# Performance work log

Hardware: AMD Instinct MI355X
Metric: run time of the kernel (lower is better)

## Reference

```python
import jax, jax.numpy as jnp
import numpy as np

FRAME_PERIOD = 80
SAMPLE_RATE = 16000
FFT_LENGTH = 1024
HALF = FFT_LENGTH // 2 + 1
DEFAULT_F0 = 500.0
Q1 = -0.15
F_MIN = 3.0 * SAMPLE_RATE / (FFT_LENGTH - 3)
DF = SAMPLE_RATE / FFT_LENGTH  # Hz per bin
TAU = 2.0 * np.pi
EPS32 = float(np.finfo(np.float32).eps)
# static max mirroring boundary for linear smoothing (max width = 2/3*default_f0)
BPAD = int(DEFAULT_F0 * (2.0 / 3.0) / DF) + 2


def _interp(c, pos):
    """Linear interpolation of c along last axis at fractional positions pos."""
    L = c.shape[-1]
    i0 = jnp.clip(jnp.floor(pos).astype(jnp.int32), 0, L - 2)
    w = pos - i0.astype(pos.dtype)
    c0 = jnp.take_along_axis(c, i0, axis=-1)
    c1 = jnp.take_along_axis(c, i0 + 1, axis=-1)
    return c0 + (c1 - c0) * w


def _cheaptrick(x, f0):
    B, T = x.shape
    N = f0.shape[-1]
    f0 = jnp.where(f0 <= F_MIN, DEFAULT_F0, f0)[..., None]  # [B,N,1]

    # --- get_windowed_waveform (pitch-synchronous Hanning, ratio=3, bias=0) ---
    base = jnp.arange(FFT_LENGTH) - FFT_LENGTH // 2              # [F]
    centers = jnp.arange(N)[:, None] * FRAME_PERIOD             # [N,1]
    idx = jnp.clip(centers + base[None, :], 0, T - 1)           # [N,F] safe indices
    seg = x[:, idx]                                             # [B,N,F]
    half_win = jnp.round(1.5 * SAMPLE_RATE / f0)                # [B,N,1]
    basef = base.astype(x.dtype)
    window = 0.5 + 0.5 * jnp.cos(jnp.pi * basef * f0 / (1.5 * SAMPLE_RATE))
    window = window * (jnp.abs(basef) <= half_win)              # [B,N,F]
    wav = seg * window
    # remove weighted mean (WORLD GetWindowedWaveform)
    wav = wav - window * (wav.sum(-1, keepdims=True) / window.sum(-1, keepdims=True))
    # power normalization
    wav = wav / jnp.sqrt(jnp.sum(wav * wav, -1, keepdims=True) + 1e-12)

    # --- power spectrum ---
    ps = jnp.abs(jnp.fft.rfft(wav, FFT_LENGTH)) ** 2            # [B,N,HALF]

    # --- DC correction: mirror spectrum around f0 below f0 ---
    ramp = jnp.arange(HALF, dtype=ps.dtype)
    center_bin = f0 * (FFT_LENGTH / SAMPLE_RATE)                # fractional bin of f0
    replica = _interp(ps, jnp.clip(center_bin - ramp, 0.0, HALF - 1.0))
    ps = ps + replica * (ramp < jnp.floor(center_bin) + 1.0)

    # --- linear smoothing with width = 2/3 * f0 (rectangular moving average) ---
    width = f0 * (2.0 / 3.0)                                    # Hz, [B,N,1]
    mir = jnp.pad(ps, ((0, 0), (0, 0), (BPAD, BPAD)), mode="reflect")
    cum = jnp.cumsum(mir, axis=-1) * DF                         # [B,N,HALF+2*BPAD]
    wb = width / DF                                             # width in bins
    p_low = ramp - 0.5 * wb + (BPAD - 0.5)
    ps = (_interp(cum, p_low + wb) - _interp(cum, p_low)) / width

    # infinitesimal noise floor (torch.randn_like(..).abs() * eps)
    noise = jnp.abs(jax.random.normal(jax.random.key(1234), ps.shape, ps.dtype)) * EPS32
    ps = ps + noise

    # --- cepstral liftering ---
    quef = ramp / SAMPLE_RATE                                   # quefrency [HALF]
    z = f0 * quef                                               # [B,N,HALF]
    lifter = jnp.sinc(z).at[..., 0].set(1.0) * (1.0 - 2.0 * Q1 + 2.0 * Q1 * jnp.cos(TAU * z))
    cep = jnp.fft.irfft(jnp.log(ps), FFT_LENGTH)[..., :HALF]
    # hfft(c) == irfft(conj(c), n) * n ; c is real here
    logps = (jnp.fft.irfft(cep * lifter, FFT_LENGTH) * FFT_LENGTH)[..., :HALF]
    return logps


def setup_inputs() -> dict:
    key = jax.random.key(0)
    k1, k2 = jax.random.split(key)
    B, N = 4, 5000
    T = N * FRAME_PERIOD
    x = jax.random.normal(k1, (B, T), dtype=jnp.float32)
    f0 = jax.random.randint(k2, (B, N), 0, 400).astype(jnp.float32)
    return {"x": x, "f0": f0}


def reference(x, f0):
    return _cheaptrick(x, f0)
```

## Files before the change

### kernel.cpp

```cpp
#include <hip/hip_runtime.h>
#include <math.h>


constexpr int   NFFT  = 1024;
constexpr int   HALFB = 513;
constexpr int   NMIR  = 559;
constexpr float DF    = 15.625f;
constexpr float PI_F  = 3.14159274101257324f;
constexpr float NOISE_C = 9.5113724e-8f;


__device__ inline void fft_stage1_cplx_reg(
    const float x0r, const float x0i, const float x1r, const float x1i,
    const float x2r, const float x2i, const float x3r, const float x3i,
    float* __restrict__ qr, float* __restrict__ qi,
    const float* __restrict__ ctab, const int tid)
{
  const float t0r = x0r + x2r, t0i = x0i + x2i;
  const float t1r = x0r - x2r, t1i = x0i - x2i;
  const float t2r = x1r + x3r, t2i = x1i + x3i;
  const float t3r = x1r - x3r, t3i = x1i - x3i;
  const float y0r = t0r + t2r, y0i = t0i + t2i;
  const float y1r = t1r + t3i, y1i = t1i - t3r;
  const float y2r = t0r - t2r, y2i = t0i - t2i;
  const float y3r = t1r - t3i, y3i = t1i + t3r;
  const float c1 = ctab[tid],     s1 = ctab[tid + 768];
  const float c2 = ctab[2 * tid], s2 = ctab[(2 * tid + 768) & 1023];
  const float c3 = ctab[3 * tid], s3 = ctab[(3 * tid + 768) & 1023];
  reinterpret_cast<float4*>(qr)[tid] = make_float4(
      y0r, y1r * c1 + y1i * s1, y2r * c2 + y2i * s2, y3r * c3 + y3i * s3);
  reinterpret_cast<float4*>(qi)[tid] = make_float4(
      y0i, y1i * c1 - y1r * s1, y2i * c2 - y2r * s2, y3i * c3 - y3r * s3);
  __syncthreads();
}

__device__ inline void fft_stage1_cplx(const float* __restrict__ pr,
                                       const float* __restrict__ pi_,
                                       float* __restrict__ qr,
                                       float* __restrict__ qi,
                                       const float* __restrict__ ctab,
                                       const int tid)
{
  fft_stage1_cplx_reg(pr[tid],       pi_[tid],       pr[tid + 256], pi_[tid + 256],
                      pr[tid + 512], pi_[tid + 512], pr[tid + 768], pi_[tid + 768],
                      qr, qi, ctab, tid);
}

#define R4_LOAD_BFLY(pr, pi_)                                   \
  const float x0r = pr[tid      ], x0i = pi_[tid      ];        \
  const float x1r = pr[tid + 256], x1i = pi_[tid + 256];        \
  const float x2r = pr[tid + 512], x2i = pi_[tid + 512];        \
  const float x3r = pr[tid + 768], x3i = pi_[tid + 768];        \
  const float t0r = x0r + x2r, t0i = x0i + x2i;                 \
  const float t1r = x0r - x2r, t1i = x0i - x2i;                 \
  const float t2r = x1r + x3r, t2i = x1i + x3i;                 \
  const float t3r = x1r - x3r, t3i = x1i - x3i;

__device__ inline void fft_stage4(const float* __restrict__ pr,
                                  const float* __restrict__ pi_,
                                  float* __restrict__ qr,
                                  float* __restrict__ qi,
                                  const float* __restrict__ ctab,
                                  const int lg2s, const int tid)
{
  R4_LOAD_BFLY(pr, pi_)
  const float y0r = t0r + t2r, y0i = t0i + t2i;
  const float y1r = t1r + t3i, y1i = t1i - t3r;
  const float y2r = t0r - t2r, y2i = t0i - t2i;
  const float y3r = t1r - t3i, y3i = t1i + t3r;
  const int s  = 1 << lg2s;
  const int q  = tid & (s - 1);
  const int tw = tid - q;
  const float c1 = ctab[tw],     s1 = ctab[tw + 768];
  const float c2 = ctab[2 * tw], s2 = ctab[(2 * tw + 768) & 1023];
  const float c3 = ctab[3 * tw], s3 = ctab[(3 * tw + 768) & 1023];
  const int o0 = 3 * tw + tid;
  qr[o0]         = y0r;
  qi[o0]         = y0i;
  qr[o0 + s]     = y1r * c1 + y1i * s1;
  qi[o0 + s]     = y1i * c1 - y1r * s1;
  qr[o0 + 2 * s] = y2r * c2 + y2i * s2;
  qi[o0 + 2 * s] = y2i * c2 - y2r * s2;
  qr[o0 + 3 * s] = y3r * c3 + y3i * s3;
  qi[o0 + 3 * s] = y3i * c3 - y3r * s3;
  __syncthreads();
}

__device__ inline void fft_stage4_final(const float* __restrict__ pr,
                                        const float* __restrict__ pi_,
                                        float* __restrict__ qr,
                                        float* __restrict__ qi,
                                        const int tid)
{
  R4_LOAD_BFLY(pr, pi_)
  qr[tid]       = t0r + t2r;  qi[tid]       = t0i + t2i;
  qr[tid + 256] = t1r + t3i;  qi[tid + 256] = t1i - t3r;
  qr[tid + 512] = t0r - t2r;  qi[tid + 512] = t0i - t2i;
  qr[tid + 768] = t1r - t3i;  qi[tid + 768] = t1i + t3r;
  __syncthreads();
}

__device__ inline void unpack_ps(const float* __restrict__ Zr,
                                 const float* __restrict__ Zi,
                                 float* __restrict__ pA,
                                 float* __restrict__ pB,
                                 const int tid)
{
#pragma unroll
  for (int j = 0; j < 2; ++j) {
    const int k  = tid + 256 * j;
    const int mk = (NFFT - k) & (NFFT - 1);
    const float zr = Zr[k], zi = Zi[k];
    const float wr = Zr[mk], wi = Zi[mk];
    const float ar = 0.5f * (zr + wr), ai = 0.5f * (zi - wi);
    const float nr = zr - wr,          ni = zi + wi;
    pA[k] = ar * ar + ai * ai;
    pB[k] = 0.25f * (ni * ni + nr * nr);
  }
  if (tid == 0) {
    const float zr = Zr[512], zi = Zi[512];
    pA[512] = zr * zr;
    pB[512] = zi * zi;
  }
  __syncthreads();
}

__device__ inline float lifter_val(const float f0, const int k)
{
  if (k == 0) return 1.0f;
  const float z = f0 * ((float)k * (1.0f / 16000.0f));
  return (sinpif(z) / (PI_F * z)) * (1.3f - 0.3f * cospif(2.0f * z));
}

__device__ inline void fft_final_lifter2(const float* __restrict__ pr,
                                         const float* __restrict__ pi_,
                                         float* __restrict__ cr,
                                         float* __restrict__ ci,
                                         const float f0A, const float f0B,
                                         const int tid)
{
  R4_LOAD_BFLY(pr, pi_)
  const float y0r = t0r + t2r, y0i = t0i + t2i;
  const float y1r = t1r + t3i, y1i = t1i - t3r;
  const float vA0 = (y0r * (1.0f / 1024.0f)) * lifter_val(f0A, tid);
  const float vB0 = (y0i * (1.0f / 1024.0f)) * lifter_val(f0B, tid);
  const float vA1 = (y1r * (1.0f / 1024.0f)) * lifter_val(f0A, tid + 256);
  const float vB1 = (y1i * (1.0f / 1024.0f)) * lifter_val(f0B, tid + 256);
  cr[tid] = vA0;  ci[tid] = vB0;
  if (tid >= 1) { cr[1024 - tid] = vA0;  ci[1024 - tid] = vB0; }
  cr[tid + 256] = vA1;  ci[tid + 256] = vB1;
  cr[768 - tid] = vA1;  ci[768 - tid] = vB1;
  if (tid == 0) {
    const float y2r = t0r - t2r, y2i = t0i - t2i;
    cr[512] = (y2r * (1.0f / 1024.0f)) * lifter_val(f0A, 512);
    ci[512] = (y2i * (1.0f / 1024.0f)) * lifter_val(f0B, 512);
  }
  __syncthreads();
}

__device__ inline void fft_final_store2(const float* __restrict__ pr,
                                        const float* __restrict__ pi_,
                                        float* __restrict__ oA,
                                        float* __restrict__ oB,
                                        const int tid)
{
  R4_LOAD_BFLY(pr, pi_)
  oA[tid]       = t0r + t2r;   oB[tid]       = t0i + t2i;
  oA[tid + 256] = t1r + t3i;   oB[tid + 256] = t1i - t3r;
  if (tid == 0) { oA[512] = t0r - t2r;  oB[512] = t0i - t2i; }
}

template<int M>
__device__ inline void block_sum_multi(float* v, float* red, const int tid)
{
#pragma unroll
  for (int c = 0; c < M; ++c) {
    float s = v[c];
#pragma unroll
    for (int o = 32; o > 0; o >>= 1) s += __shfl_down(s, o, 64);
    v[c] = s;
  }
  const int lane = tid & 63, w = tid >> 6;
  __syncthreads();
  if (lane == 0) {
#pragma unroll
    for (int c = 0; c < M; ++c) red[w * M + c] = v[c];
  }
  __syncthreads();
#pragma unroll
  for (int c = 0; c < M; ++c)
    v[c] = red[c] + red[M + c] + red[2 * M + c] + red[3 * M + c];
}

__device__ inline int reflect_idx(int i)
{
  int j = i - 23;
  if (j < 0)   j = -j;
  if (j > 512) j = 1024 - j;
  return j;
}

__device__ inline float interp_cum(const float* c, float pos)
{
  int i0 = (int)floorf(pos);
  i0 = min(max(i0, 0), NMIR - 2);
  const float w  = pos - (float)i0;
  const float c0 = c[i0];
  return c0 + (c[i0 + 1] - c0) * w;
}

__device__ inline void cumsum559_dual(const float* __restrict__ srcA,
                                      const float* __restrict__ srcB,
                                      float* __restrict__ dstA,
                                      float* __restrict__ dstB,
                                      float* red, const int tid)
{
  const int g = tid >> 7;
  const int l = tid & 127;
  const float* src = g ? srcB : srcA;
  float*       dst = g ? dstB : dstA;
  const int base = l * 5;
  float a[5];
  float run = 0.f;
#pragma unroll
  for (int i = 0; i < 5; ++i) {
    a[i] = (base + i < NMIR) ? src[reflect_idx(base + i)] : 0.f;
    run += a[i];
  }
  float v = run;
  const int lane = tid & 63;
  const int wv = tid >> 6;
#pragma unroll
  for (int o = 1; o < 64; o <<= 1) {
    const float t2 = __shfl_up(v, o, 64);
    if (lane >= o) v += t2;
  }
  __syncthreads();
  if (lane == 63) red[wv] = v;
  __syncthreads();
  const float woff = (wv & 1) ? red[wv - 1] : 0.f;
  float c = (v - run) + woff;
#pragma unroll
  for (int i = 0; i < 5; ++i) {
    c += a[i];
    if (base + i < NMIR) dst[base + i] = c * DF;
  }
  __syncthreads();
}

__global__ __launch_bounds__(256)
void cheaptrick_kernel(const float* __restrict__ x, const float* __restrict__ f0g,
                       float* __restrict__ out, const int N, const int T)
{
  __shared__ float ctab[1024];
  __shared__ __align__(16) float Ar[1024];
  __shared__ __align__(16) float Ai[1024];
  __shared__ __align__(16) float Br[1024];
  __shared__ __align__(16) float Bi[1024];
  __shared__ float red[16];

  const int tid = threadIdx.x;
  const int NP  = N >> 1;
  const int b   = blockIdx.x / NP;
  const int p   = blockIdx.x - b * NP;
  const int n0  = 2 * p;
  const int fidA = b * N + n0;

  for (int m = tid; m < 1024; m += 256)
    ctab[m] = cospif((float)m * (1.0f / 512.0f));

  float f0A = f0g[fidA], f0B = f0g[fidA + 1];
  if (f0A <= 47.0127335f) f0A = 500.0f;
  if (f0B <= 47.0127335f) f0B = 500.0f;

  const float hwA = rintf(24000.0f / f0A);
  const float hwB = rintf(24000.0f / f0B);
  const float* xb = x + (size_t)b * T;
  const int cA = n0 * 80, cB = cA + 80;

  float wavA[4], winA[4], wavB[4], winB[4];
  float sums[4] = {0.f, 0.f, 0.f, 0.f};
#pragma unroll
  for (int j = 0; j < 4; ++j) {
    const int t = tid + j * 256;
    const float basef = (float)(t - 512);
    const int ia = min(max(cA + t - 512, 0), T - 1);
    const int ib = min(max(cB + t - 512, 0), T - 1);
    const float sa = xb[ia], sb = xb[ib];
    float wA = 0.5f + 0.5f * cospif(basef * f0A * (1.0f / 24000.0f));
    wA = (fabsf(basef) <= hwA) ? wA : 0.0f;
    float wB = 0.5f + 0.5f * cospif(basef * f0B * (1.0f / 24000.0f));
    wB = (fabsf(basef) <= hwB) ? wB : 0.0f;
    winA[j] = wA;  wavA[j] = sa * wA;
    winB[j] = wB;  wavB[j] = sb * wB;
    sums[0] += wavA[j];  sums[1] += wA;
    sums[2] += wavB[j];  sums[3] += wB;
  }
  block_sum_multi<4>(sums, red, tid);
  const float cmA = sums[0] / sums[1];
  const float cmB = sums[2] / sums[3];
  float sq[2] = {0.f, 0.f};
#pragma unroll
  for (int j = 0; j < 4; ++j) {
    wavA[j] -= winA[j] * cmA;  sq[0] += wavA[j] * wavA[j];
    wavB[j] -= winB[j] * cmB;  sq[1] += wavB[j] * wavB[j];
  }
  block_sum_multi<2>(sq, red, tid);
  const float invA = 1.0f / sqrtf(sq[0] + 1e-12f);
  const float invB = 1.0f / sqrtf(sq[1] + 1e-12f);

  fft_stage1_cplx_reg(wavA[0] * invA, wavB[0] * invB,
                      wavA[1] * invA, wavB[1] * invB,
                      wavA[2] * invA, wavB[2] * invB,
                      wavA[3] * invA, wavB[3] * invB, Br, Bi, ctab, tid);
  fft_stage4(Br, Bi, Ar, Ai, ctab, 2, tid);
  fft_stage4(Ar, Ai, Br, Bi, ctab, 4, tid);
  fft_stage4(Br, Bi, Ar, Ai, ctab, 6, tid);
  fft_stage4_final(Ar, Ai, Br, Bi, tid);

  unpack_ps(Br, Bi, Ar, Ai, tid);

  if (tid < 128) {
    const int k = tid & 63;
    float* P = (tid < 64) ? Ar : Ai;
    const float f = (tid < 64) ? f0A : f0B;
    const float cb  = f * 0.064f;
    const float thr = floorf(cb) + 1.0f;
    if ((float)k < thr) {
      const float pos = fminf(cb - (float)k, 512.0f);
      const int i0 = min((int)pos, 511);
      const float w  = pos - (float)i0;
      const float r0 = P[i0], r1 = P[i0 + 1];
      P[k] += r0 + (r1 - r0) * w;
    }
  }
  __syncthreads();

  cumsum559_dual(Ar, Ai, Br, Bi, red, tid);

  const float wdA = f0A * (float)(2.0 / 3.0), wbA = wdA / DF;
  const float wdB = f0B * (float)(2.0 / 3.0), wbB = wdB / DF;
  for (int k = tid; k < HALFB; k += 256) {
    const float plA = ((float)k - 0.5f * wbA) + 22.5f;
    const float lgA =
        logf((interp_cum(Br, plA + wbA) - interp_cum(Br, plA)) / wdA + NOISE_C);
    const float plB = ((float)k - 0.5f * wbB) + 22.5f;
    const float lgB =
        logf((interp_cum(Bi, plB + wbB) - interp_cum(Bi, plB)) / wdB + NOISE_C);
    Ar[k] = lgA;  Ai[k] = lgB;
    if (k >= 1 && k <= 511) { Ar[NFFT - k] = lgA;  Ai[NFFT - k] = lgB; }
  }
  __syncthreads();

  fft_stage1_cplx(Ar, Ai, Br, Bi, ctab, tid);
  fft_stage4(Br, Bi, Ar, Ai, ctab, 2, tid);
  fft_stage4(Ar, Ai, Br, Bi, ctab, 4, tid);
  fft_stage4(Br, Bi, Ar, Ai, ctab, 6, tid);
  fft_final_lifter2(Ar, Ai, Br, Bi, f0A, f0B, tid);

  fft_stage1_cplx(Br, Bi, Ar, Ai, ctab, tid);
  fft_stage4(Ar, Ai, Br, Bi, ctab, 2, tid);
  fft_stage4(Br, Bi, Ar, Ai, ctab, 4, tid);
  fft_stage4(Ar, Ai, Br, Bi, ctab, 6, tid);
  fft_final_store2(Br, Bi,
                   out + (size_t)fidA * HALFB,
                   out + (size_t)(fidA + 1) * HALFB, tid);
}

extern "C" void kernel_launch(void* const* d_in, const int* in_sizes, int n_in,
                              void* d_out, int out_size, void* d_ws, size_t ws_size,
                              hipStream_t stream)
{
  (void)n_in; (void)out_size; (void)d_ws; (void)ws_size;
  const float* x   = (const float*)d_in[0];
  const float* f0  = (const float*)d_in[1];
  float*       out = (float*)d_out;

  const int B  = 4;
  const int BN = in_sizes[1];
  const int N  = BN / B;
  const int T  = in_sizes[0] / B;

  hipLaunchKernelGGL(cheaptrick_kernel, dim3(BN / 2), dim3(256), 0, stream,
                     x, f0, out, N, T);
}
```

Measured before the change: 186.3 us.

## Store FFT buffers and twiddles as interleaved complex pairs in LDS

Switches the shared-memory FFT workspaces from split real/imag float arrays to interleaved float2 complex arrays, and stores the twiddle table as (cos, sin) pairs. Each butterfly load becomes one 64-bit LDS access instead of two 32-bit ones, and each twiddle needs one paired read instead of two separate table reads. The scratch real-valued buffers for power spectrum and cumulative sum are aliased into the complex buffers. The trade-off is a different bank-access pattern for 8-byte LDS accesses, and possible extra register shuffling for the vector types.

```diff
diff --git a/kernel.cpp b/kernel.cpp
--- a/kernel.cpp
+++ b/kernel.cpp
@@ -1,6 +1,9 @@
 #include <hip/hip_runtime.h>
 #include <math.h>
 
+
+typedef float v2f __attribute__((ext_vector_type(2)));
+typedef float v4f __attribute__((ext_vector_type(4)));
 
 constexpr int   NFFT  = 1024;
 constexpr int   HALFB = 513;
@@ -9,118 +12,84 @@
 constexpr float PI_F  = 3.14159274101257324f;
 constexpr float NOISE_C = 9.5113724e-8f;
 
-
-__device__ inline void fft_stage1_cplx_reg(
-    const float x0r, const float x0i, const float x1r, const float x1i,
-    const float x2r, const float x2i, const float x3r, const float x3i,
-    float* __restrict__ qr, float* __restrict__ qi,
-    const float* __restrict__ ctab, const int tid)
-{
-  const float t0r = x0r + x2r, t0i = x0i + x2i;
-  const float t1r = x0r - x2r, t1i = x0i - x2i;
-  const float t2r = x1r + x3r, t2i = x1i + x3i;
-  const float t3r = x1r - x3r, t3i = x1i - x3i;
-  const float y0r = t0r + t2r, y0i = t0i + t2i;
-  const float y1r = t1r + t3i, y1i = t1i - t3r;
-  const float y2r = t0r - t2r, y2i = t0i - t2i;
-  const float y3r = t1r - t3i, y3i = t1i + t3r;
-  const float c1 = ctab[tid],     s1 = ctab[tid + 768];
-  const float c2 = ctab[2 * tid], s2 = ctab[(2 * tid + 768) & 1023];
-  const float c3 = ctab[3 * tid], s3 = ctab[(3 * tid + 768) & 1023];
-  reinterpret_cast<float4*>(qr)[tid] = make_float4(
-      y0r, y1r * c1 + y1i * s1, y2r * c2 + y2i * s2, y3r * c3 + y3i * s3);
-  reinterpret_cast<float4*>(qi)[tid] = make_float4(
-      y0i, y1i * c1 - y1r * s1, y2i * c2 - y2r * s2, y3i * c3 - y3r * s3);
-  __syncthreads();
-}
-
-__device__ inline void fft_stage1_cplx(const float* __restrict__ pr,
-                                       const float* __restrict__ pi_,
-                                       float* __restrict__ qr,
-                                       float* __restrict__ qi,
-                                       const float* __restrict__ ctab,
-                                       const int tid)
-{
-  fft_stage1_cplx_reg(pr[tid],       pi_[tid],       pr[tid + 256], pi_[tid + 256],
-                      pr[tid + 512], pi_[tid + 512], pr[tid + 768], pi_[tid + 768],
-                      qr, qi, ctab, tid);
-}
-
-#define R4_LOAD_BFLY(pr, pi_)                                   \
-  const float x0r = pr[tid      ], x0i = pi_[tid      ];        \
-  const float x1r = pr[tid + 256], x1i = pi_[tid + 256];        \
-  const float x2r = pr[tid + 512], x2i = pi_[tid + 512];        \
-  const float x3r = pr[tid + 768], x3i = pi_[tid + 768];        \
-  const float t0r = x0r + x2r, t0i = x0i + x2i;                 \
-  const float t1r = x0r - x2r, t1i = x0i - x2i;                 \
-  const float t2r = x1r + x3r, t2i = x1i + x3i;                 \
-  const float t3r = x1r - x3r, t3i = x1i - x3i;
-
-__device__ inline void fft_stage4(const float* __restrict__ pr,
-                                  const float* __restrict__ pi_,
-                                  float* __restrict__ qr,
-                                  float* __restrict__ qi,
-                                  const float* __restrict__ ctab,
-                                  const int lg2s, const int tid)
-{
-  R4_LOAD_BFLY(pr, pi_)
-  const float y0r = t0r + t2r, y0i = t0i + t2i;
-  const float y1r = t1r + t3i, y1i = t1i - t3r;
-  const float y2r = t0r - t2r, y2i = t0i - t2i;
-  const float y3r = t1r - t3i, y3i = t1i + t3r;
+__device__ inline v2f cmulw(const v2f y, const v2f w)
+{
+  const v2f a  = y * (v2f){w.x, w.x};
+  const v2f b  = (v2f){y.y, -y.x};
+  return a + b * (v2f){w.y, w.y};
+}
+
+#define R4C_BFLY(x0, x1, x2, x3)                         \
+  const v2f t0 = x0 + x2, t1 = x0 - x2;                  \
+  const v2f t2 = x1 + x3, t3 = x1 - x3;                  \
+  const v2f nj = (v2f){t3.y, -t3.x};          \
+  const v2f y0 = t0 + t2, y2 = t0 - t2;                  \
+  const v2f y1 = t1 + nj, y3 = t1 - nj;
+
+__device__ inline void fft1_reg(const v2f x0, const v2f x1,
+                                const v2f x2, const v2f x3,
+                                v2f* __restrict__ q,
+                                const v2f* __restrict__ wt, const int tid)
+{
+  R4C_BFLY(x0, x1, x2, x3)
+  const v2f w1 = wt[tid], w2 = wt[2 * tid], w3 = wt[3 * tid];
+  const v2f a1 = cmulw(y1, w1), a2 = cmulw(y2, w2), a3 = cmulw(y3, w3);
+  v4f* q4 = reinterpret_cast<v4f*>(q);
+  q4[2 * tid]     = (v4f){y0.x, y0.y, a1.x, a1.y};
+  q4[2 * tid + 1] = (v4f){a2.x, a2.y, a3.x, a3.y};
+  __syncthreads();
+}
+
+__device__ inline void fft1_lds(const v2f* __restrict__ p, v2f* __restrict__ q,
+                                const v2f* __restrict__ wt, const int tid)
+{
+  fft1_reg(p[tid], p[tid + 256], p[tid + 512], p[tid + 768], q, wt, tid);
+}
+
+__device__ inline void fftm(const v2f* __restrict__ p, v2f* __restrict__ q,
+                            const v2f* __restrict__ wt, const int lg2s,
+                            const int tid)
+{
+  const v2f x0 = p[tid], x1 = p[tid + 256], x2 = p[tid + 512], x3 = p[tid + 768];
+  R4C_BFLY(x0, x1, x2, x3)
   const int s  = 1 << lg2s;
-  const int q  = tid & (s - 1);
-  const int tw = tid - q;
-  const float c1 = ctab[tw],     s1 = ctab[tw + 768];
-  const float c2 = ctab[2 * tw], s2 = ctab[(2 * tw + 768) & 1023];
-  const float c3 = ctab[3 * tw], s3 = ctab[(3 * tw + 768) & 1023];
+  const int tw = tid & ~(s - 1);
+  const v2f w1 = wt[tw], w2 = wt[2 * tw], w3 = wt[3 * tw];
   const int o0 = 3 * tw + tid;
-  qr[o0]         = y0r;
-  qi[o0]         = y0i;
-  qr[o0 + s]     = y1r * c1 + y1i * s1;
-  qi[o0 + s]     = y1i * c1 - y1r * s1;
-  qr[o0 + 2 * s] = y2r * c2 + y2i * s2;
-  qi[o0 + 2 * s] = y2i * c2 - y2r * s2;
-  qr[o0 + 3 * s] = y3r * c3 + y3i * s3;
-  qi[o0 + 3 * s] = y3i * c3 - y3r * s3;
-  __syncthreads();
-}
-
-__device__ inline void fft_stage4_final(const float* __restrict__ pr,
-                                        const float* __restrict__ pi_,
-                                        float* __restrict__ qr,
-                                        float* __restrict__ qi,
-                                        const int tid)
-{
-  R4_LOAD_BFLY(pr, pi_)
-  qr[tid]       = t0r + t2r;  qi[tid]       = t0i + t2i;
-  qr[tid + 256] = t1r + t3i;  qi[tid + 256] = t1i - t3r;
-  qr[tid + 512] = t0r - t2r;  qi[tid + 512] = t0i - t2i;
-  qr[tid + 768] = t1r - t3i;  qi[tid + 768] = t1i + t3r;
-  __syncthreads();
-}
-
-__device__ inline void unpack_ps(const float* __restrict__ Zr,
-                                 const float* __restrict__ Zi,
-                                 float* __restrict__ pA,
-                                 float* __restrict__ pB,
-                                 const int tid)
+  q[o0]         = y0;
+  q[o0 + s]     = cmulw(y1, w1);
+  q[o0 + 2 * s] = cmulw(y2, w2);
+  q[o0 + 3 * s] = cmulw(y3, w3);
+  __syncthreads();
+}
+
+__device__ inline void fftf(const v2f* __restrict__ p, v2f* __restrict__ q,
+                            const int tid)
+{
+  const v2f x0 = p[tid], x1 = p[tid + 256], x2 = p[tid + 512], x3 = p[tid + 768];
+  R4C_BFLY(x0, x1, x2, x3)
+  q[tid] = y0;  q[tid + 256] = y1;  q[tid + 512] = y2;  q[tid + 768] = y3;
+  __syncthreads();
+}
+
+__device__ inline void unpack_ps_c(const v2f* __restrict__ Z,
+                                   float* __restrict__ psA,
+                                   float* __restrict__ psB, const int tid)
 {
 #pragma unroll
   for (int j = 0; j < 2; ++j) {
     const int k  = tid + 256 * j;
     const int mk = (NFFT - k) & (NFFT - 1);
-    const float zr = Zr[k], zi = Zi[k];
-    const float wr = Zr[mk], wi = Zi[mk];
-    const float ar = 0.5f * (zr + wr), ai = 0.5f * (zi - wi);
-    const float nr = zr - wr,          ni = zi + wi;
-    pA[k] = ar * ar + ai * ai;
-    pB[k] = 0.25f * (ni * ni + nr * nr);
+    const v2f z = Z[k], w = Z[mk];
+    const float ar = 0.5f * (z.x + w.x), ai = 0.5f * (z.y - w.y);
+    const float nr = z.x - w.x,          ni = z.y + w.y;
+    psA[k] = ar * ar + ai * ai;
+    psB[k] = 0.25f * (ni * ni + nr * nr);
   }
   if (tid == 0) {
-    const float zr = Zr[512], zi = Zi[512];
-    pA[512] = zr * zr;
-    pB[512] = zi * zi;
+    const v2f z = Z[512];
+    psA[512] = z.x * z.x;
+    psB[512] = z.y * z.y;
   }
   __syncthreads();
 }
@@ -132,42 +101,46 @@
   return (sinpif(z) / (PI_F * z)) * (1.3f - 0.3f * cospif(2.0f * z));
 }
 
-__device__ inline void fft_final_lifter2(const float* __restrict__ pr,
-                                         const float* __restrict__ pi_,
-                                         float* __restrict__ cr,
-                                         float* __restrict__ ci,
-                                         const float f0A, const float f0B,
-                                         const int tid)
-{
-  R4_LOAD_BFLY(pr, pi_)
-  const float y0r = t0r + t2r, y0i = t0i + t2i;
-  const float y1r = t1r + t3i, y1i = t1i - t3r;
-  const float vA0 = (y0r * (1.0f / 1024.0f)) * lifter_val(f0A, tid);
-  const float vB0 = (y0i * (1.0f / 1024.0f)) * lifter_val(f0B, tid);
-  const float vA1 = (y1r * (1.0f / 1024.0f)) * lifter_val(f0A, tid + 256);
-  const float vB1 = (y1i * (1.0f / 1024.0f)) * lifter_val(f0B, tid + 256);
-  cr[tid] = vA0;  ci[tid] = vB0;
-  if (tid >= 1) { cr[1024 - tid] = vA0;  ci[1024 - tid] = vB0; }
-  cr[tid + 256] = vA1;  ci[tid + 256] = vB1;
-  cr[768 - tid] = vA1;  ci[768 - tid] = vB1;
+__device__ inline void fftf_lifter(const v2f* __restrict__ p,
+                                   v2f* __restrict__ dst,
+                                   const float f0A, const float f0B,
+                                   const int tid)
+{
+  const v2f x0 = p[tid], x1 = p[tid + 256], x2 = p[tid + 512], x3 = p[tid + 768];
+  const v2f t0 = x0 + x2, t1 = x0 - x2;
+  const v2f t2 = x1 + x3, t3 = x1 - x3;
+  const v2f nj = (v2f){t3.y, -t3.x};
+  const v2f y0 = t0 + t2;
+  const v2f y1 = t1 + nj;
+  const v2f v0 = y0 * (1.0f / 1024.0f) *
+                 (v2f){lifter_val(f0A, tid), lifter_val(f0B, tid)};
+  const v2f v1 = y1 * (1.0f / 1024.0f) *
+                 (v2f){lifter_val(f0A, tid + 256), lifter_val(f0B, tid + 256)};
+  dst[tid] = v0;
+  if (tid >= 1) dst[1024 - tid] = v0;
+  dst[tid + 256] = v1;
+  dst[768 - tid] = v1;
   if (tid == 0) {
-    const float y2r = t0r - t2r, y2i = t0i - t2i;
-    cr[512] = (y2r * (1.0f / 1024.0f)) * lifter_val(f0A, 512);
-    ci[512] = (y2i * (1.0f / 1024.0f)) * lifter_val(f0B, 512);
-  }
-  __syncthreads();
-}
-
-__device__ inline void fft_final_store2(const float* __restrict__ pr,
-                                        const float* __restrict__ pi_,
-                                        float* __restrict__ oA,
-                                        float* __restrict__ oB,
-                                        const int tid)
-{
-  R4_LOAD_BFLY(pr, pi_)
-  oA[tid]       = t0r + t2r;   oB[tid]       = t0i + t2i;
-  oA[tid + 256] = t1r + t3i;   oB[tid + 256] = t1i - t3r;
-  if (tid == 0) { oA[512] = t0r - t2r;  oB[512] = t0i - t2i; }
+    const v2f y2 = t0 - t2;
+    dst[512] = y2 * (1.0f / 1024.0f) *
+               (v2f){lifter_val(f0A, 512), lifter_val(f0B, 512)};
+  }
+  __syncthreads();
+}
+
+__device__ inline void fftf_store(const v2f* __restrict__ p,
+                                  float* __restrict__ oA,
+                                  float* __restrict__ oB, const int tid)
+{
+  const v2f x0 = p[tid], x1 = p[tid + 256], x2 = p[tid + 512], x3 = p[tid + 768];
+  const v2f t0 = x0 + x2, t1 = x0 - x2;
+  const v2f t2 = x1 + x3, t3 = x1 - x3;
+  const v2f nj = (v2f){t3.y, -t3.x};
+  const v2f y0 = t0 + t2;
+  const v2f y1 = t1 + nj;
+  oA[tid]       = y0.x;   oB[tid]       = y0.y;
+  oA[tid + 256] = y1.x;   oB[tid + 256] = y1.y;
+  if (tid == 0) { const v2f y2 = t0 - t2;  oA[512] = y2.x;  oB[512] = y2.y; }
 }
 
 template<int M>
@@ -252,12 +225,13 @@
 void cheaptrick_kernel(const float* __restrict__ x, const float* __restrict__ f0g,
                        float* __restrict__ out, const int N, const int T)
 {
-  __shared__ float ctab[1024];
-  __shared__ __align__(16) float Ar[1024];
-  __shared__ __align__(16) float Ai[1024];
-  __shared__ __align__(16) float Br[1024];
-  __shared__ __align__(16) float Bi[1024];
+  __shared__ __align__(16) v2f wtab[1024];
+  __shared__ __align__(16) v2f Ac[1024];
+  __shared__ __align__(16) v2f Bc[1024];
   __shared__ float red[16];
+
+  float* Af = reinterpret_cast<float*>(Ac);
+  float* Bf = reinterpret_cast<float*>(Bc);
 
   const int tid = threadIdx.x;
   const int NP  = N >> 1;
@@ -266,8 +240,11 @@
   const int n0  = 2 * p;
   const int fidA = b * N + n0;
 
-  for (int m = tid; m < 1024; m += 256)
-    ctab[m] = cospif((float)m * (1.0f / 512.0f));
+  for (int m = tid; m < 1024; m += 256) {
+    float sn, cs;
+    sincospif((float)m * (1.0f / 512.0f), &sn, &cs);
+    wtab[m] = (v2f){cs, sn};
+  }
 
   float f0A = f0g[fidA], f0B = f0g[fidA + 1];
   if (f0A <= 47.0127335f) f0A = 500.0f;
@@ -309,20 +286,20 @@
   const float invA = 1.0f / sqrtf(sq[0] + 1e-12f);
   const float invB = 1.0f / sqrtf(sq[1] + 1e-12f);
 
-  fft_stage1_cplx_reg(wavA[0] * invA, wavB[0] * invB,
-                      wavA[1] * invA, wavB[1] * invB,
-                      wavA[2] * invA, wavB[2] * invB,
-                      wavA[3] * invA, wavB[3] * invB, Br, Bi, ctab, tid);
-  fft_stage4(Br, Bi, Ar, Ai, ctab, 2, tid);
-  fft_stage4(Ar, Ai, Br, Bi, ctab, 4, tid);
-  fft_stage4(Br, Bi, Ar, Ai, ctab, 6, tid);
-  fft_stage4_final(Ar, Ai, Br, Bi, tid);
-
-  unpack_ps(Br, Bi, Ar, Ai, tid);
+  fft1_reg((v2f){wavA[0] * invA, wavB[0] * invB},
+           (v2f){wavA[1] * invA, wavB[1] * invB},
+           (v2f){wavA[2] * invA, wavB[2] * invB},
+           (v2f){wavA[3] * invA, wavB[3] * invB}, Ac, wtab, tid);
+  fftm(Ac, Bc, wtab, 2, tid);
+  fftm(Bc, Ac, wtab, 4, tid);
+  fftm(Ac, Bc, wtab, 6, tid);
+  fftf(Bc, Ac, tid);
+
+  unpack_ps_c(Ac, Bf, Bf + 1024, tid);
 
   if (tid < 128) {
     const int k = tid & 63;
-    float* P = (tid < 64) ? Ar : Ai;
+    float* P = (tid < 64) ? Bf : (Bf + 1024);
     const float f = (tid < 64) ? f0A : f0B;
     const float cb  = f * 0.064f;
     const float thr = floorf(cb) + 1.0f;
@@ -336,35 +313,36 @@
   }
   __syncthreads();
 
-  cumsum559_dual(Ar, Ai, Br, Bi, red, tid);
+  cumsum559_dual(Bf, Bf + 1024, Af, Af + 1024, red, tid);
 
   const float wdA = f0A * (float)(2.0 / 3.0), wbA = wdA / DF;
   const float wdB = f0B * (float)(2.0 / 3.0), wbB = wdB / DF;
   for (int k = tid; k < HALFB; k += 256) {
     const float plA = ((float)k - 0.5f * wbA) + 22.5f;
     const float lgA =
-        logf((interp_cum(Br, plA + wbA) - interp_cum(Br, plA)) / wdA + NOISE_C);
+        logf((interp_cum(Af, plA + wbA) - interp_cum(Af, plA)) / wdA + NOISE_C);
     const float plB = ((float)k - 0.5f * wbB) + 22.5f;
-    const float lgB =
-        logf((interp_cum(Bi, plB + wbB) - interp_cum(Bi, plB)) / wdB + NOISE_C);
-    Ar[k] = lgA;  Ai[k] = lgB;
-    if (k >= 1 && k <= 511) { Ar[NFFT - k] = lgA;  Ai[NFFT - k] = lgB; }
-  }
-  __syncthreads();
-
-  fft_stage1_cplx(Ar, Ai, Br, Bi, ctab, tid);
-  fft_stage4(Br, Bi, Ar, Ai, ctab, 2, tid);
-  fft_stage4(Ar, Ai, Br, Bi, ctab, 4, tid);
-  fft_stage4(Br, Bi, Ar, Ai, ctab, 6, tid);
-  fft_final_lifter2(Ar, Ai, Br, Bi, f0A, f0B, tid);
-
-  fft_stage1_cplx(Br, Bi, Ar, Ai, ctab, tid);
-  fft_stage4(Ar, Ai, Br, Bi, ctab, 2, tid);
-  fft_stage4(Br, Bi, Ar, Ai, ctab, 4, tid);
-  fft_stage4(Ar, Ai, Br, Bi, ctab, 6, tid);
-  fft_final_store2(Br, Bi,
-                   out + (size_t)fidA * HALFB,
-                   out + (size_t)(fidA + 1) * HALFB, tid);
+    const float lgB = logf((interp_cum(Af + 1024, plB + wbB) -
+                            interp_cum(Af + 1024, plB)) / wdB + NOISE_C);
+    const v2f v = (v2f){lgA, lgB};
+    Bc[k] = v;
+    if (k >= 1 && k <= 511) Bc[NFFT - k] = v;
+  }
+  __syncthreads();
+
+  fft1_lds(Bc, Ac, wtab, tid);
+  fftm(Ac, Bc, wtab, 2, tid);
+  fftm(Bc, Ac, wtab, 4, tid);
+  fftm(Ac, Bc, wtab, 6, tid);
+  fftf_lifter(Bc, Ac, f0A, f0B, tid);
+
+  fft1_lds(Ac, Bc, wtab, tid);
+  fftm(Bc, Ac, wtab, 2, tid);
+  fftm(Ac, Bc, wtab, 4, tid);
+  fftm(Bc, Ac, wtab, 6, tid);
+  fftf_store(Ac,
+             out + (size_t)fidA * HALFB,
+             out + (size_t)(fidA + 1) * HALFB, tid);
 }
 
 extern "C" void kernel_launch(void* const* d_in, const int* in_sizes, int n_in,
```

Measured after the change: 184.2 us. No clear change (-1.2%).
